# Kernel optimization log

Measured on AMD Instinct MI355X. Metric: run time of the kernel, lower is better.

The kernel has to match this reference:

```python
import jax, jax.numpy as jnp
import numpy as np

B, S, D = 2, 11253, 256
NHEAD, NLEVEL, DFF = 8, 4, 1024
KERNEL = 2
NPOINT = KERNEL * KERNEL
HEAD_DIM = D // NHEAD
LEVEL_SHAPES = [(92, 92), (46, 46), (23, 23), (12, 12)]
LEVEL_STARTS = np.cumsum([0] + [h * w for h, w in LEVEL_SHAPES])[:-1]


def _kernel_indices():
    # BoxeR _create_kernel_indices: even kernel -> [-0.5, 0.5]/K, (x, y) order
    idx = np.arange(KERNEL, dtype=np.float32) - (KERNEL - 1) / 2.0
    i, j = np.meshgrid(idx, idx, indexing="ij")
    return jnp.asarray(np.stack([j, i], -1).reshape(-1, 2) / KERNEL)


KIDX = _kernel_indices()  # (NPOINT, 2) box-relative sample offsets


def layer_norm(x, w, b, eps=1e-5):
    mu = x.mean(-1, keepdims=True)
    var = ((x - mu) ** 2).mean(-1, keepdims=True)
    return (x - mu) * jax.lax.rsqrt(var + eps) * w + b


def setup_inputs() -> dict:
    key = jax.random.key(0)
    ks = jax.random.split(key, 12)

    def p(i, shape, scale=0.02):
        return jax.random.normal(ks[i], shape, jnp.float32) * scale

    cxcy = jax.random.uniform(ks[2], (B, S, 2), jnp.float32, minval=0.1, maxval=0.9)
    wh = jax.random.uniform(ks[3], (B, S, 2), jnp.float32, minval=0.02, maxval=0.2)
    return dict(
        src=jax.random.normal(ks[0], (B, S, D), jnp.float32),
        pos=jax.random.normal(ks[1], (B, S, D), jnp.float32),
        src_shape=jnp.asarray(np.array(LEVEL_SHAPES, np.int32)),
        src_mask=jnp.zeros((B, S), jnp.bool_),
        src_start_index=jnp.asarray(LEVEL_STARTS.astype(np.int32)),
        src_valid_ratios=jnp.ones((B, NLEVEL, 2), jnp.float32),
        ref_windows=jnp.concatenate([cxcy, wh], -1),
        value_w=p(4, (D, D)), value_b=jnp.zeros((D,), jnp.float32),
        out_w=p(5, (D, D)), out_b=jnp.zeros((D,), jnp.float32),
        box_w=p(6, (NHEAD * NLEVEL * 4, D)), box_b=jnp.zeros((NHEAD * NLEVEL * 4,), jnp.float32),
        attn_w=p(7, (NHEAD * NLEVEL * NPOINT, D)), attn_b=jnp.zeros((NHEAD * NLEVEL * NPOINT,), jnp.float32),
        lin1_w=p(8, (DFF, D)), lin1_b=jnp.zeros((DFF,), jnp.float32),
        lin2_w=p(9, (D, DFF)), lin2_b=jnp.zeros((D,), jnp.float32),
        norm1_w=jnp.ones((D,), jnp.float32), norm1_b=jnp.zeros((D,), jnp.float32),
        norm2_w=jnp.ones((D,), jnp.float32), norm2_b=jnp.zeros((D,), jnp.float32),
    )


def box_attention(q, src, src_mask, src_valid_ratios, ref_windows,
                  value_w, value_b, out_w, out_b, box_w, box_b, attn_w, attn_b):
    value = src @ value_w.T + value_b
    value = jnp.where(src_mask[..., None], 0.0, value)
    value = value.reshape(B, S, NHEAD, HEAD_DIM)

    # where-to-attend: per-head, per-level box offsets decoded around ref_windows (cx,cy,w,h)
    off = (q @ box_w.T + box_b).reshape(B, S, NHEAD, NLEVEL, 4)
    ref = ref_windows[:, :, None, None, :]
    boxes = ref + off / 8.0 * ref[..., jnp.array([2, 3, 2, 3])]
    center, size = boxes[..., None, :2], boxes[..., None, 2:]
    grid = center + KIDX * jax.nn.relu(size)  # (B,S,nh,L,P,2) in normalized [0,1] coords
    grid = grid * src_valid_ratios[:, None, None, :, None, :]

    attn = (q @ attn_w.T + attn_b).reshape(B, S, NHEAD, NLEVEL * NPOINT)
    attn = jax.nn.softmax(attn, -1).reshape(B, S, NHEAD, NLEVEL, NPOINT)

    out = jnp.zeros((B, NHEAD, S, HEAD_DIM), src.dtype)
    for lvl, (H, W) in enumerate(LEVEL_SHAPES):
        s0 = int(LEVEL_STARTS[lvl])
        v = jnp.transpose(value[:, s0:s0 + H * W], (0, 2, 1, 3))  # (B,nh,HW,hd)
        loc = jnp.transpose(grid[:, :, :, lvl], (0, 2, 1, 3, 4))  # (B,nh,S,P,2)
        # grid_sample bilinear, align_corners=False, zero padding
        px = loc[..., 0] * W - 0.5
        py = loc[..., 1] * H - 0.5
        x0, y0 = jnp.floor(px), jnp.floor(py)
        wx, wy = (px - x0)[..., None], (py - y0)[..., None]

        def gather(ix, iy):
            valid = (ix >= 0) & (ix < W) & (iy >= 0) & (iy < H)
            idx = (jnp.clip(iy, 0, H - 1) * W + jnp.clip(ix, 0, W - 1)).astype(jnp.int32)
            g = jnp.take_along_axis(v, idx.reshape(B, NHEAD, S * NPOINT)[..., None], axis=2)
            return g.reshape(B, NHEAD, S, NPOINT, HEAD_DIM) * valid[..., None]

        g00, g01 = gather(x0, y0), gather(x0 + 1, y0)
        g10, g11 = gather(x0, y0 + 1), gather(x0 + 1, y0 + 1)
        samp = (g00 * (1 - wx) + g01 * wx) * (1 - wy) + (g10 * (1 - wx) + g11 * wx) * wy
        aw = jnp.transpose(attn[:, :, :, lvl], (0, 2, 1, 3))  # (B,nh,S,P)
        out = out + jnp.einsum("bhspd,bhsp->bhsd", samp, aw)

    out = jnp.transpose(out, (0, 2, 1, 3)).reshape(B, S, D)
    return out @ out_w.T + out_b


def reference(src, pos, src_shape, src_mask, src_start_index, src_valid_ratios,
              ref_windows, value_w, value_b, out_w, out_b, box_w, box_b,
              attn_w, attn_b, lin1_w, lin1_b, lin2_w, lin2_b,
              norm1_w, norm1_b, norm2_w, norm2_b):
    # self-attn (box attention) + residual + LN
    src2 = box_attention(src + pos, src, src_mask, src_valid_ratios, ref_windows,
                         value_w, value_b, out_w, out_b, box_w, box_b, attn_w, attn_b)
    x = layer_norm(src + src2, norm1_w, norm1_b)
    # FFN + residual + LN (dropout=0 in eval)
    ff = jax.nn.relu(x @ lin1_w.T + lin1_b) @ lin2_w.T + lin2_b
    return layer_norm(x + ff, norm2_w, norm2_b)
```

## Files before the change

kernel.cpp:

```cpp
#include <hip/hip_runtime.h>
#include <hip/hip_bf16.h>
#include <hip/hip_fp16.h>

#define TOKENS 22506
#define SLEN   11253

typedef __bf16 bf16x8 __attribute__((ext_vector_type(8)));
typedef float  f32x4  __attribute__((ext_vector_type(4)));
typedef float  f32x2  __attribute__((ext_vector_type(2)));
typedef uint   u32x4  __attribute__((ext_vector_type(4)));

#if defined(__has_builtin)
#if __has_builtin(__builtin_amdgcn_cvt_pk_f32_fp8) && __has_builtin(__builtin_amdgcn_cvt_pk_fp8_f32)
#define HAS_FP8CVT 1
#endif
#endif

__device__ __forceinline__ ushort f2bu(float f) {
    __hip_bfloat16 h = __float2bfloat16(f);
    return *reinterpret_cast<ushort*>(&h);
}
__device__ __forceinline__ float bu2f(ushort u) {
    return __uint_as_float((uint)u << 16);
}
__device__ __forceinline__ uint pkf16(float a, float b) {
    __half2 h = __floats2half2_rn(a, b);
    return *reinterpret_cast<uint*>(&h);
}
__device__ __forceinline__ void gl16(const ushort* g, ushort* l) {
    __builtin_amdgcn_global_load_lds(
        (__attribute__((address_space(1))) void*)(g),
        (__attribute__((address_space(3))) void*)(l), 16, 0, 0);
}

#ifndef HAS_FP8CVT
__device__ __forceinline__ uint enc_fp8(float x) {
    if (!(fabsf(x) >= 0.f)) return 0;
    uint u = __float_as_uint(x);
    uint s = (u >> 24) & 0x80u;
    float ax = fabsf(x);
    if (ax >= 448.f) return s | 0x7Eu;
    if (ax < 0.0009765625f) return s;
    int e; frexpf(ax, &e);
    int ue = e - 1;
    if (ue < -6) {
        int m = (int)(ax * 512.f + 0.5f);
        if (m > 7) m = 7;
        return s | (uint)m;
    }
    float q = ax * exp2f((float)(3 - ue));
    int mi = (int)(q + 0.5f);
    if (mi >= 16) { mi >>= 1; ++ue; if (ue > 8) return s | 0x7Eu; }
    return s | ((uint)(ue + 7) << 3) | ((uint)mi & 7u);
}
__device__ __forceinline__ float dec_fp8(uint b) {
    const float sgn = (b & 0x80u) ? -1.f : 1.f;
    const uint e = (b >> 3) & 15u, m = b & 7u;
    if (e == 0) return sgn * (float)m * 0.001953125f;
    return sgn * (1.0f + (float)m * 0.125f) * exp2f((float)e - 7.f);
}
#endif

__device__ __forceinline__ uint fp8pack4(float f0, float f1, float f2, float f3) {
#ifdef HAS_FP8CVT
    int p = 0;
    p = __builtin_amdgcn_cvt_pk_fp8_f32(f0, f1, p, false);
    p = __builtin_amdgcn_cvt_pk_fp8_f32(f2, f3, p, true);
    return (uint)p;
#else
    return enc_fp8(f0) | (enc_fp8(f1) << 8) | (enc_fp8(f2) << 16) | (enc_fp8(f3) << 24);
#endif
}
template<bool HI>
__device__ __forceinline__ f32x2 fp8pair(uint w) {
#ifdef HAS_FP8CVT
    auto c = __builtin_amdgcn_cvt_pk_f32_fp8((int)w, HI);
    f32x2 r; r.x = c[0]; r.y = c[1]; return r;
#else
    const uint sh = HI ? 16u : 0u;
    f32x2 r; r.x = dec_fp8((w >> sh) & 0xFFu); r.y = dec_fp8((w >> (sh + 8)) & 0xFFu);
    return r;
#endif
}

template<bool RELU, bool NTSTORE, bool F8Z0>
__global__ __launch_bounds__(256) void gemm_small(
    const ushort* __restrict__ A0, const ushort* __restrict__ W0,
    const float* __restrict__ b0, void* __restrict__ C0,
    const ushort* __restrict__ A1, const ushort* __restrict__ W1,
    const float* __restrict__ b1, void* __restrict__ C1,
    int M, int N, int K)
{
    const bool zz = blockIdx.z != 0;
    const ushort* A   = zz ? A1 : A0;
    const ushort* W   = zz ? W1 : W0;
    const float* bias = zz ? b1 : b0;
    void* Cptr        = zz ? C1 : C0;

    __shared__ ushort smem[12288];
    const int tid  = threadIdx.x;
    const int lane = tid & 63;
    const int wid  = tid >> 6;
    const int wr = wid >> 1, wc = wid & 1;
    const int m0 = blockIdx.x * 64, n0 = blockIdx.y * 128;
    const int lrow = lane & 15, lhi = lane >> 4;

    const int arow = tid >> 2;
    const int scol = (tid & 3) << 3;
    const ushort* ga  = A + (size_t)min(m0 + arow, M - 1) * K + scol;
    const ushort* gb0 = W + (size_t)(n0 + arow)      * K + scol;
    const ushort* gb1 = W + (size_t)(n0 + arow + 64) * K + scol;

    f32x4 acc[2][4] = {};
    const int NT = K >> 5;

    gl16(ga,  &smem[tid * 8]);
    gl16(gb0, &smem[4096 + tid * 8]);
    gl16(gb1, &smem[4096 + tid * 8 + 2048]);

    int cur = 0;
    for (int t = 0; t < NT; ++t) {
        __syncthreads();
        if (t + 1 < NT) {
            const int k0 = (t + 1) << 5;
            const int nb = cur ^ 1;
            gl16(ga  + k0, &smem[nb * 2048 + tid * 8]);
            gl16(gb0 + k0, &smem[4096 + nb * 4096 + tid * 8]);
            gl16(gb1 + k0, &smem[4096 + nb * 4096 + tid * 8 + 2048]);
        }
        bf16x8 afr[2], bfr[4];
        #pragma unroll
        for (int m = 0; m < 2; ++m)
            afr[m] = *reinterpret_cast<const bf16x8*>(
                &smem[cur * 2048 + (wr * 32 + m * 16 + lrow) * 32 + lhi * 8]);
        #pragma unroll
        for (int n = 0; n < 4; ++n)
            bfr[n] = *reinterpret_cast<const bf16x8*>(
                &smem[4096 + cur * 4096 + (wc * 64 + n * 16 + lrow) * 32 + lhi * 8]);
        #pragma unroll
        for (int m = 0; m < 2; ++m)
            #pragma unroll
            for (int n = 0; n < 4; ++n)
                acc[m][n] = __builtin_amdgcn_mfma_f32_16x16x32_bf16(
                    afr[m], bfr[n], acc[m][n], 0, 0, 0);
        cur ^= 1;
    }

    __syncthreads();
    #pragma unroll
    for (int m = 0; m < 2; ++m) {
        #pragma unroll
        for (int n = 0; n < 4; ++n) {
            const int col = wc * 64 + n * 16 + lrow;
            const float bv = bias[n0 + col];
            #pragma unroll
            for (int r = 0; r < 4; ++r) {
                const int row = wr * 32 + m * 16 + lhi * 4 + r;
                float v = acc[m][n][r] + bv;
                if (RELU) v = fmaxf(v, 0.f);
                smem[row * 136 + col] = f2bu(v);
            }
        }
    }
    __syncthreads();
    if (F8Z0 && !zz) {
        #pragma unroll
        for (int i = 0; i < 4; ++i) {
            const int e = tid + i * 256;
            const int row = e >> 4, ch = e & 15;
            if (m0 + row < M) {
                const u32x4 v = *reinterpret_cast<const u32x4*>(&smem[row * 136 + ch * 8]);
                float f[8];
                #pragma unroll
                for (int j = 0; j < 4; ++j) {
                    f[2 * j]     = __uint_as_float(v[j] << 16);
                    f[2 * j + 1] = __uint_as_float(v[j] & 0xFFFF0000u);
                }
                uint2 o;
                o.x = fp8pack4(f[0], f[1], f[2], f[3]);
                o.y = fp8pack4(f[4], f[5], f[6], f[7]);
                *reinterpret_cast<uint2*>(
                    (unsigned char*)Cptr + (size_t)(m0 + row) * N + n0 + ch * 8) = o;
            }
        }
    } else {
        #pragma unroll
        for (int i = 0; i < 4; ++i) {
            const int e = tid + i * 256;
            const int row = e >> 4, ch = e & 15;
            if (m0 + row < M) {
                const u32x4 v = *reinterpret_cast<const u32x4*>(&smem[row * 136 + ch * 8]);
                u32x4* dst = reinterpret_cast<u32x4*>(
                    (ushort*)Cptr + (size_t)(m0 + row) * N + n0 + ch * 8);
                if (NTSTORE) __builtin_nontemporal_store(v, dst);
                else *dst = v;
            }
        }
    }
}

__global__ __launch_bounds__(256) void prep_all(
    const float* __restrict__ vw, const float* __restrict__ bw,
    const float* __restrict__ aw, const float* __restrict__ ow,
    const float* __restrict__ l1, const float* __restrict__ l2,
    const float* __restrict__ bb, const float* __restrict__ ab,
    ushort* __restrict__ dstW, float* __restrict__ dstQB,
    const float4* __restrict__ src, const float4* __restrict__ pos,
    ushort4* __restrict__ srcb, ushort4* __restrict__ qb)
{
    const int blk = blockIdx.x;
    if (blk < 2817) {
        const int i = blk * 256 + threadIdx.x;
        if (i < 720896) {
            float v;
            if      (i <  65536) v = vw[i];
            else if (i <  98304) v = bw[i -  65536];
            else if (i < 131072) v = aw[i -  98304];
            else if (i < 196608) v = ow[i - 131072];
            else if (i < 458752) v = l1[i - 196608];
            else                 v = l2[i - 458752];
            dstW[i] = f2bu(v);
        } else if (i < 721152) {
            const int j = i - 720896;
            dstQB[j] = (j < 128) ? bb[j] : ab[j - 128];
        }
    } else {
        const int i = (blk - 2817) * 256 + threadIdx.x;
        if (i >= TOKENS * 64) return;
        const float4 s = src[i], p = pos[i];
        ushort4 us, uq;
        us.x = f2bu(s.x); us.y = f2bu(s.y); us.z = f2bu(s.z); us.w = f2bu(s.w);
        uq.x = f2bu(s.x + p.x); uq.y = f2bu(s.y + p.y);
        uq.z = f2bu(s.z + p.z); uq.w = f2bu(s.w + p.w);
        srcb[i] = us; qb[i] = uq;
    }
}

__global__ __launch_bounds__(256) void box_fused(
    const unsigned char* __restrict__ val,
    const ushort* __restrict__ qout,
    const float* __restrict__ refw,
    const float* __restrict__ vratio,
    ushort* __restrict__ attnout)
{
    __shared__ ushort4 offs[64 * 17];
    __shared__ uint2 wts[64 * 17];
    const int tid = threadIdx.x;
    const int t0 = blockIdx.x * 8;

    {
        const int u = tid >> 2, lvl = tid & 3;
        const int t = min(t0 + (u >> 3), TOKENS - 1);
        const int h = u & 7;
        const int b = (t >= SLEN) ? 1 : 0;
        const ushort* qr = qout + (size_t)t * 256;

        const uint2 lu = *reinterpret_cast<const uint2*>(qr + 128 + h * 16 + lvl * 4);
        float e0 = __uint_as_float(lu.x << 16);
        float e1 = __uint_as_float(lu.x & 0xFFFF0000u);
        float e2 = __uint_as_float(lu.y << 16);
        float e3 = __uint_as_float(lu.y & 0xFFFF0000u);
        float mx = fmaxf(fmaxf(e0, e1), fmaxf(e2, e3));
        mx = fmaxf(mx, __shfl_xor(mx, 1));
        mx = fmaxf(mx, __shfl_xor(mx, 2));
        e0 = __expf(e0 - mx); e1 = __expf(e1 - mx);
        e2 = __expf(e2 - mx); e3 = __expf(e3 - mx);
        float ss = e0 + e1 + e2 + e3;
        ss += __shfl_xor(ss, 1);
        ss += __shfl_xor(ss, 2);
        const float inv = 1.f / ss;
        const float pe[4] = { e0 * inv, e1 * inv, e2 * inv, e3 * inv };

        const uint2 ou = *reinterpret_cast<const uint2*>(qr + h * 16 + lvl * 4);
        const float o0 = __uint_as_float(ou.x << 16) * 0.125f;
        const float o1 = __uint_as_float(ou.x & 0xFFFF0000u) * 0.125f;
        const float o2 = __uint_as_float(ou.y << 16) * 0.125f;
        const float o3 = __uint_as_float(ou.y & 0xFFFF0000u) * 0.125f;

        const float4 rw = *reinterpret_cast<const float4*>(refw + (size_t)t * 4);
        const int Ww = (lvl == 0) ? 92 : (lvl == 1) ? 46 : (lvl == 2) ? 23 : 12;
        const int s0 = (lvl == 0) ? 0 : (lvl == 1) ? 8464 : (lvl == 2) ? 10580 : 11109;
        const float vrx = vratio[(b * 4 + lvl) * 2 + 0];
        const float vry = vratio[(b * 4 + lvl) * 2 + 1];

        const float bx  = rw.x + o0 * rw.z;
        const float by  = rw.y + o1 * rw.w;
        const float bwd = fmaxf(rw.z + o2 * rw.z, 0.f);
        const float bhd = fmaxf(rw.w + o3 * rw.w, 0.f);

        #pragma unroll
        for (int k = 0; k < 4; ++k) {
            const float jx = (k & 1) ? 0.25f : -0.25f;
            const float iy = (k & 2) ? 0.25f : -0.25f;
            const float px = (bx + jx * bwd) * vrx * (float)Ww - 0.5f;
            const float py = (by + iy * bhd) * vry * (float)Ww - 0.5f;
            const float x0f = floorf(px), y0f = floorf(py);
            const int x0 = (int)x0f, y0 = (int)y0f;
            const float wx = px - x0f, wy = py - y0f;
            const float wp = pe[k];

            const bool vx0 = (x0 >= 0) && (x0 < Ww);
            const bool vx1 = (x0 + 1 >= 0) && (x0 + 1 < Ww);
            const bool vy0 = (y0 >= 0) && (y0 < Ww);
            const bool vy1 = (y0 + 1 >= 0) && (y0 + 1 < Ww);
            const int cx0 = min(max(x0, 0), Ww - 1);
            const int cx1 = min(max(x0 + 1, 0), Ww - 1);
            const int cy0 = min(max(y0, 0), Ww - 1);
            const int cy1 = min(max(y0 + 1, 0), Ww - 1);

            const float w00 = (vx0 && vy0) ? wp * (1.f - wx) * (1.f - wy) : 0.f;
            const float w01 = (vx1 && vy0) ? wp * wx         * (1.f - wy) : 0.f;
            const float w10 = (vx0 && vy1) ? wp * (1.f - wx) * wy         : 0.f;
            const float w11 = (vx1 && vy1) ? wp * wx         * wy         : 0.f;

            ushort4 sp;
            sp.x = (ushort)(s0 + cy0 * Ww + cx0);
            sp.y = (ushort)(s0 + cy0 * Ww + cx1);
            sp.z = (ushort)(s0 + cy1 * Ww + cx0);
            sp.w = (ushort)(s0 + cy1 * Ww + cx1);

            const int p = lvl * 4 + k;
            offs[u * 17 + p] = sp;
            wts[u * 17 + p]  = make_uint2(pkf16(w00, w01), pkf16(w10, w11));
        }
    }
    __syncthreads();

    const int u = tid >> 2, dl = tid & 3;
    const int traw = t0 + (u >> 3);
    const int t = min(traw, TOKENS - 1);
    const int h = u & 7;
    const uint boff = ((t >= SLEN) ? (uint)SLEN * 256u : 0u) + (uint)h * 32u + (uint)dl * 8u;
    const char* base = (const char*)val;

    const ushort4* po = &offs[u * 17];
    const uint2* pw = &wts[u * 17];
    f32x2 a0 = {0.f, 0.f}, a1 = {0.f, 0.f}, a2 = {0.f, 0.f}, a3 = {0.f, 0.f};

    #pragma unroll
    for (int g = 0; g < 8; ++g) {
        const ushort4 sA = po[g * 2 + 0];
        const ushort4 sB = po[g * 2 + 1];
        const uint2 wA = pw[g * 2 + 0];
        const uint2 wB = pw[g * 2 + 1];

        const uint2 v0 = *reinterpret_cast<const uint2*>(base + (((uint)sA.x << 8) + boff));
        const uint2 v1 = *reinterpret_cast<const uint2*>(base + (((uint)sA.y << 8) + boff));
        const uint2 v2 = *reinterpret_cast<const uint2*>(base + (((uint)sA.z << 8) + boff));
        const uint2 v3 = *reinterpret_cast<const uint2*>(base + (((uint)sA.w << 8) + boff));
        const uint2 v4 = *reinterpret_cast<const uint2*>(base + (((uint)sB.x << 8) + boff));
        const uint2 v5 = *reinterpret_cast<const uint2*>(base + (((uint)sB.y << 8) + boff));
        const uint2 v6 = *reinterpret_cast<const uint2*>(base + (((uint)sB.z << 8) + boff));
        const uint2 v7 = *reinterpret_cast<const uint2*>(base + (((uint)sB.w << 8) + boff));

        const float2 wAl = __half22float2(*reinterpret_cast<const __half2*>(&wA.x));
        const float2 wAh = __half22float2(*reinterpret_cast<const __half2*>(&wA.y));
        const float2 wBl = __half22float2(*reinterpret_cast<const __half2*>(&wB.x));
        const float2 wBh = __half22float2(*reinterpret_cast<const __half2*>(&wB.y));

        auto accf8 = [&](const uint2 v, const float w) {
            f32x2 wv; wv.x = w; wv.y = w;
            a0 += wv * fp8pair<false>(v.x);
            a1 += wv * fp8pair<true>(v.x);
            a2 += wv * fp8pair<false>(v.y);
            a3 += wv * fp8pair<true>(v.y);
        };
        accf8(v0, wAl.x); accf8(v1, wAl.y); accf8(v2, wAh.x); accf8(v3, wAh.y);
        accf8(v4, wBl.x); accf8(v5, wBl.y); accf8(v6, wBh.x); accf8(v7, wBh.y);
    }

    if (traw < TOKENS) {
        u32x4 o;
        o[0] = (uint)f2bu(a0.x) | ((uint)f2bu(a0.y) << 16);
        o[1] = (uint)f2bu(a1.x) | ((uint)f2bu(a1.y) << 16);
        o[2] = (uint)f2bu(a2.x) | ((uint)f2bu(a2.y) << 16);
        o[3] = (uint)f2bu(a3.x) | ((uint)f2bu(a3.y) << 16);
        *reinterpret_cast<u32x4*>(attnout + (size_t)t * 256 + h * 32 + dl * 8) = o;
    }
}

template<bool AF32, bool OUTF32>
__global__ __launch_bounds__(256) void ln_add2(
    const void* __restrict__ aptr, const ushort* __restrict__ bptr,
    const float* __restrict__ w, const float* __restrict__ bias,
    void* __restrict__ outp, int nrows)
{
    const int lane = threadIdx.x & 63, wv = threadIdx.x >> 6;
    const int row = blockIdx.x * 4 + wv;
    if (row >= nrows) return;
    const size_t base = (size_t)row * 256 + lane * 4;

    float4 av;
    if (AF32) {
        av = *reinterpret_cast<const float4*>((const float*)aptr + base);
    } else {
        const ushort4 u = *reinterpret_cast<const ushort4*>((const ushort*)aptr + base);
        av = make_float4(bu2f(u.x), bu2f(u.y), bu2f(u.z), bu2f(u.w));
    }
    const ushort4 ub = *reinterpret_cast<const ushort4*>(bptr + base);
    const float v0 = av.x + bu2f(ub.x), v1 = av.y + bu2f(ub.y);
    const float v2 = av.z + bu2f(ub.z), v3 = av.w + bu2f(ub.w);

    float s = v0 + v1 + v2 + v3;
    #pragma unroll
    for (int o = 32; o; o >>= 1) s += __shfl_xor(s, o);
    const float mu = s * (1.f / 256.f);
    const float d0 = v0 - mu, d1 = v1 - mu, d2 = v2 - mu, d3 = v3 - mu;
    float s2 = d0 * d0 + d1 * d1 + d2 * d2 + d3 * d3;
    #pragma unroll
    for (int o = 32; o; o >>= 1) s2 += __shfl_xor(s2, o);
    const float rs = rsqrtf(s2 * (1.f / 256.f) + 1e-5f);

    const float4 w4 = *reinterpret_cast<const float4*>(w + lane * 4);
    const float4 g4 = *reinterpret_cast<const float4*>(bias + lane * 4);
    const float r0 = d0 * rs * w4.x + g4.x;
    const float r1 = d1 * rs * w4.y + g4.y;
    const float r2 = d2 * rs * w4.z + g4.z;
    const float r3 = d3 * rs * w4.w + g4.w;
    if (OUTF32) {
        *reinterpret_cast<float4*>((float*)outp + base) = make_float4(r0, r1, r2, r3);
    } else {
        ushort4 u;
        u.x = f2bu(r0); u.y = f2bu(r1); u.z = f2bu(r2); u.w = f2bu(r3);
        *reinterpret_cast<ushort4*>((ushort*)outp + base) = u;
    }
}

extern "C" void kernel_launch(void* const* d_in, const int* in_sizes, int n_in,
                              void* d_out, int out_size, void* d_ws, size_t ws_size,
                              hipStream_t stream)
{
    const float* src     = (const float*)d_in[0];
    const float* pos     = (const float*)d_in[1];
    const float* vratio  = (const float*)d_in[5];
    const float* refw    = (const float*)d_in[6];
    const float* value_w = (const float*)d_in[7];
    const float* value_b = (const float*)d_in[8];
    const float* out_w   = (const float*)d_in[9];
    const float* out_b   = (const float*)d_in[10];
    const float* box_w   = (const float*)d_in[11];
    const float* box_b   = (const float*)d_in[12];
    const float* attn_w  = (const float*)d_in[13];
    const float* attn_b  = (const float*)d_in[14];
    const float* lin1_w  = (const float*)d_in[15];
    const float* lin1_b  = (const float*)d_in[16];
    const float* lin2_w  = (const float*)d_in[17];
    const float* lin2_b  = (const float*)d_in[18];
    const float* n1w     = (const float*)d_in[19];
    const float* n1b     = (const float*)d_in[20];
    const float* n2w     = (const float*)d_in[21];
    const float* n2b     = (const float*)d_in[22];

    char* wsb = (char*)d_ws;
    ushort* Wb    = (ushort*)(wsb);
    float*  qcb   = (float*)(wsb + 1441792);
    ushort* srcb  = (ushort*)(wsb + 1442816);
    ushort* qb    = (ushort*)(wsb + 12965888);
    unsigned char* valb = (unsigned char*)(wsb + 24488960);
    ushort* qoutb = (ushort*)(wsb + 36012032);
    ushort* attb  = (ushort*)(wsb + 47535104);
    ushort* src2b = (ushort*)(wsb + 59058176);
    ushort* xbb   = (ushort*)(wsb + 70581248);
    ushort* hb    = (ushort*)(wsb + 82104320);
    ushort* yb    = (ushort*)(wsb + 128196608);

    const dim3 blk(256);

    prep_all<<<dim3(8444), blk, 0, stream>>>(
        value_w, box_w, attn_w, out_w, lin1_w, lin2_w, box_b, attn_b, Wb, qcb,
        (const float4*)src, (const float4*)pos, (ushort4*)srcb, (ushort4*)qb);

    gemm_small<false, false, true><<<dim3(352, 2, 2), blk, 0, stream>>>(
        srcb, Wb, value_b, valb,
        qb, Wb + 65536, qcb, qoutb, TOKENS, 256, 256);

    box_fused<<<dim3((TOKENS + 7) / 8), blk, 0, stream>>>(
        valb, qoutb, refw, vratio, attb);

    gemm_small<false, false, false><<<dim3(352, 2, 1), blk, 0, stream>>>(
        attb, Wb + 131072, out_b, src2b,
        attb, Wb + 131072, out_b, src2b, TOKENS, 256, 256);
    ln_add2<true, false><<<dim3((TOKENS + 3) / 4), blk, 0, stream>>>(
        src, src2b, n1w, n1b, xbb, TOKENS);
    gemm_small<true, true, false><<<dim3(352, 8, 1), blk, 0, stream>>>(
        xbb, Wb + 196608, lin1_b, hb,
        xbb, Wb + 196608, lin1_b, hb, TOKENS, 1024, 256);
    gemm_small<false, false, false><<<dim3(352, 2, 1), blk, 0, stream>>>(
        hb, Wb + 458752, lin2_b, yb,
        hb, Wb + 458752, lin2_b, yb, TOKENS, 256, 1024);
    ln_add2<false, true><<<dim3((TOKENS + 3) / 4), blk, 0, stream>>>(
        xbb, yb, n2w, n2b, (float*)d_out, TOKENS);
}
```

Measured before the change: 134.9 us.

## Fuse output and FFN2 GEMMs with residual add and LayerNorm

Adds a gemm_ln kernel that computes a full 256-column row tile (32 rows per block) and then, in the same kernel, applies bias, residual add and LayerNorm before storing. It replaces the out-projection GEMM plus ln_add2 and the lin2 GEMM plus ln_add2. This removes two kernel launches and the round trips of the src2 and y intermediates through global memory. In exchange each block does more serial work with a smaller M tile and fewer blocks (about 704 versus 704 blocks split over N), and the bf16 rounding of the GEMM output before LayerNorm is kept.

```diff
diff --git a/kernel.cpp b/kernel.cpp
--- a/kernel.cpp
+++ b/kernel.cpp
@@ -195,6 +195,123 @@
                 if (NTSTORE) __builtin_nontemporal_store(v, dst);
                 else *dst = v;
             }
+        }
+    }
+}
+
+template<bool RESF32, bool OUTF32>
+__global__ __launch_bounds__(256) void gemm_ln(
+    const ushort* __restrict__ A, const ushort* __restrict__ W,
+    const float* __restrict__ bias, const void* __restrict__ resid,
+    const float* __restrict__ lnw, const float* __restrict__ lnb,
+    void* __restrict__ outp, int M, int K)
+{
+    __shared__ ushort smem[18432];
+    const int tid  = threadIdx.x;
+    const int lane = tid & 63;
+    const int wid  = tid >> 6;
+    const int m0 = blockIdx.x * 32;
+    const int lrow = lane & 15, lhi = lane >> 4;
+
+    const int arow = tid >> 2;
+    const int achk = (tid & 3) << 3;
+    const ushort* ga = A + (size_t)min(m0 + (arow & 31), M - 1) * K + achk;
+    const ushort* gb = W + (size_t)arow * K + achk;
+    const size_t gstride = (size_t)64 * K;
+
+    f32x4 acc[2][4] = {};
+    const int NT = K >> 5;
+
+    if (tid < 128) gl16(ga, &smem[tid * 8]);
+    #pragma unroll
+    for (int i = 0; i < 4; ++i)
+        gl16(gb + i * gstride, &smem[2048 + (tid + i * 256) * 8]);
+
+    int cur = 0;
+    for (int t = 0; t < NT; ++t) {
+        __syncthreads();
+        if (t + 1 < NT) {
+            const int k0 = (t + 1) << 5;
+            const int nb = cur ^ 1;
+            if (tid < 128) gl16(ga + k0, &smem[nb * 1024 + tid * 8]);
+            #pragma unroll
+            for (int i = 0; i < 4; ++i)
+                gl16(gb + k0 + i * gstride, &smem[2048 + nb * 8192 + (tid + i * 256) * 8]);
+        }
+        bf16x8 afr[2], bfr[4];
+        #pragma unroll
+        for (int m = 0; m < 2; ++m)
+            afr[m] = *reinterpret_cast<const bf16x8*>(
+                &smem[cur * 1024 + (m * 16 + lrow) * 32 + lhi * 8]);
+        #pragma unroll
+        for (int n = 0; n < 4; ++n)
+            bfr[n] = *reinterpret_cast<const bf16x8*>(
+                &smem[2048 + cur * 8192 + (wid * 64 + n * 16 + lrow) * 32 + lhi * 8]);
+        #pragma unroll
+        for (int m = 0; m < 2; ++m)
+            #pragma unroll
+            for (int n = 0; n < 4; ++n)
+                acc[m][n] = __builtin_amdgcn_mfma_f32_16x16x32_bf16(
+                    afr[m], bfr[n], acc[m][n], 0, 0, 0);
+        cur ^= 1;
+    }
+
+    __syncthreads();
+    #pragma unroll
+    for (int m = 0; m < 2; ++m) {
+        #pragma unroll
+        for (int n = 0; n < 4; ++n) {
+            const int col = wid * 64 + n * 16 + lrow;
+            const float bv = bias[col];
+            #pragma unroll
+            for (int r = 0; r < 4; ++r) {
+                const int row = m * 16 + lhi * 4 + r;
+                smem[row * 264 + col] = f2bu(acc[m][n][r] + bv);
+            }
+        }
+    }
+    __syncthreads();
+
+    const float4 w4 = *reinterpret_cast<const float4*>(lnw + lane * 4);
+    const float4 g4 = *reinterpret_cast<const float4*>(lnb + lane * 4);
+    #pragma unroll
+    for (int rr = 0; rr < 8; ++rr) {
+        const int row = wid * 8 + rr;
+        const int grow = m0 + row;
+        if (grow >= M) break;
+        const size_t base = (size_t)grow * 256 + lane * 4;
+
+        const ushort4 c4 = *reinterpret_cast<const ushort4*>(&smem[row * 264 + lane * 4]);
+        float4 rv;
+        if (RESF32) {
+            rv = *reinterpret_cast<const float4*>((const float*)resid + base);
+        } else {
+            const ushort4 u = *reinterpret_cast<const ushort4*>((const ushort*)resid + base);
+            rv = make_float4(bu2f(u.x), bu2f(u.y), bu2f(u.z), bu2f(u.w));
+        }
+        const float v0 = rv.x + bu2f(c4.x), v1 = rv.y + bu2f(c4.y);
+        const float v2 = rv.z + bu2f(c4.z), v3 = rv.w + bu2f(c4.w);
+
+        float s = v0 + v1 + v2 + v3;
+        #pragma unroll
+        for (int o = 32; o; o >>= 1) s += __shfl_xor(s, o);
+        const float mu = s * (1.f / 256.f);
+        const float d0 = v0 - mu, d1 = v1 - mu, d2 = v2 - mu, d3 = v3 - mu;
+        float s2 = d0 * d0 + d1 * d1 + d2 * d2 + d3 * d3;
+        #pragma unroll
+        for (int o = 32; o; o >>= 1) s2 += __shfl_xor(s2, o);
+        const float rs = rsqrtf(s2 * (1.f / 256.f) + 1e-5f);
+
+        const float r0 = d0 * rs * w4.x + g4.x;
+        const float r1 = d1 * rs * w4.y + g4.y;
+        const float r2 = d2 * rs * w4.z + g4.z;
+        const float r3 = d3 * rs * w4.w + g4.w;
+        if (OUTF32) {
+            *reinterpret_cast<float4*>((float*)outp + base) = make_float4(r0, r1, r2, r3);
+        } else {
+            ushort4 u;
+            u.x = f2bu(r0); u.y = f2bu(r1); u.z = f2bu(r2); u.w = f2bu(r3);
+            *reinterpret_cast<ushort4*>((ushort*)outp + base) = u;
         }
     }
 }
@@ -379,53 +496,6 @@
     }
 }
 
-template<bool AF32, bool OUTF32>
-__global__ __launch_bounds__(256) void ln_add2(
-    const void* __restrict__ aptr, const ushort* __restrict__ bptr,
-    const float* __restrict__ w, const float* __restrict__ bias,
-    void* __restrict__ outp, int nrows)
-{
-    const int lane = threadIdx.x & 63, wv = threadIdx.x >> 6;
-    const int row = blockIdx.x * 4 + wv;
-    if (row >= nrows) return;
-    const size_t base = (size_t)row * 256 + lane * 4;
-
-    float4 av;
-    if (AF32) {
-        av = *reinterpret_cast<const float4*>((const float*)aptr + base);
-    } else {
-        const ushort4 u = *reinterpret_cast<const ushort4*>((const ushort*)aptr + base);
-        av = make_float4(bu2f(u.x), bu2f(u.y), bu2f(u.z), bu2f(u.w));
-    }
-    const ushort4 ub = *reinterpret_cast<const ushort4*>(bptr + base);
-    const float v0 = av.x + bu2f(ub.x), v1 = av.y + bu2f(ub.y);
-    const float v2 = av.z + bu2f(ub.z), v3 = av.w + bu2f(ub.w);
-
-    float s = v0 + v1 + v2 + v3;
-    #pragma unroll
-    for (int o = 32; o; o >>= 1) s += __shfl_xor(s, o);
-    const float mu = s * (1.f / 256.f);
-    const float d0 = v0 - mu, d1 = v1 - mu, d2 = v2 - mu, d3 = v3 - mu;
-    float s2 = d0 * d0 + d1 * d1 + d2 * d2 + d3 * d3;
-    #pragma unroll
-    for (int o = 32; o; o >>= 1) s2 += __shfl_xor(s2, o);
-    const float rs = rsqrtf(s2 * (1.f / 256.f) + 1e-5f);
-
-    const float4 w4 = *reinterpret_cast<const float4*>(w + lane * 4);
-    const float4 g4 = *reinterpret_cast<const float4*>(bias + lane * 4);
-    const float r0 = d0 * rs * w4.x + g4.x;
-    const float r1 = d1 * rs * w4.y + g4.y;
-    const float r2 = d2 * rs * w4.z + g4.z;
-    const float r3 = d3 * rs * w4.w + g4.w;
-    if (OUTF32) {
-        *reinterpret_cast<float4*>((float*)outp + base) = make_float4(r0, r1, r2, r3);
-    } else {
-        ushort4 u;
-        u.x = f2bu(r0); u.y = f2bu(r1); u.z = f2bu(r2); u.w = f2bu(r3);
-        *reinterpret_cast<ushort4*>((ushort*)outp + base) = u;
-    }
-}
-
 extern "C" void kernel_launch(void* const* d_in, const int* in_sizes, int n_in,
                               void* d_out, int out_size, void* d_ws, size_t ws_size,
                               hipStream_t stream)
@@ -459,10 +529,8 @@
     unsigned char* valb = (unsigned char*)(wsb + 24488960);
     ushort* qoutb = (ushort*)(wsb + 36012032);
     ushort* attb  = (ushort*)(wsb + 47535104);
-    ushort* src2b = (ushort*)(wsb + 59058176);
     ushort* xbb   = (ushort*)(wsb + 70581248);
     ushort* hb    = (ushort*)(wsb + 82104320);
-    ushort* yb    = (ushort*)(wsb + 128196608);
 
     const dim3 blk(256);
 
@@ -477,17 +545,13 @@
     box_fused<<<dim3((TOKENS + 7) / 8), blk, 0, stream>>>(
         valb, qoutb, refw, vratio, attb);
 
-    gemm_small<false, false, false><<<dim3(352, 2, 1), blk, 0, stream>>>(
-        attb, Wb + 131072, out_b, src2b,
-        attb, Wb + 131072, out_b, src2b, TOKENS, 256, 256);
-    ln_add2<true, false><<<dim3((TOKENS + 3) / 4), blk, 0, stream>>>(
-        src, src2b, n1w, n1b, xbb, TOKENS);
+    gemm_ln<true, false><<<dim3((TOKENS + 31) / 32), blk, 0, stream>>>(
+        attb, Wb + 131072, out_b, src, n1w, n1b, xbb, TOKENS, 256);
+
     gemm_small<true, true, false><<<dim3(352, 8, 1), blk, 0, stream>>>(
         xbb, Wb + 196608, lin1_b, hb,
         xbb, Wb + 196608, lin1_b, hb, TOKENS, 1024, 256);
-    gemm_small<false, false, false><<<dim3(352, 2, 1), blk, 0, stream>>>(
-        hb, Wb + 458752, lin2_b, yb,
-        hb, Wb + 458752, lin2_b, yb, TOKENS, 256, 1024);
-    ln_add2<false, true><<<dim3((TOKENS + 3) / 4), blk, 0, stream>>>(
-        xbb, yb, n2w, n2b, (float*)d_out, TOKENS);
-}
+
+    gemm_ln<false, true><<<dim3((TOKENS + 31) / 32), blk, 0, stream>>>(
+        hb, Wb + 458752, lin2_b, xbb, n2w, n2b, (float*)d_out, TOKENS, 1024);
+}
```

Result: slower. 143.9 us (+6.6%).
